# Performance work log

Measured on AMD Instinct MI355X. Metric: run time of the kernel, lower is better.

The kernel has to match this reference:

```python
import jax, jax.numpy as jnp
import numpy as np

B, L, D, H1, OUT, MAX_W = 16, 128, 768, 770, 40, 30


def _span_mask():
    # valid spans: i <= j and width < MAX_W (structured sparsity over the L x L grid)
    ii, jj = np.meshgrid(np.arange(L), np.arange(L), indexing='ij')
    return ((jj >= ii) & (jj - ii < MAX_W)).astype(np.int32)


def setup_inputs():
    key = jax.random.key(0)
    ks = jax.random.split(key, 5)
    hidden_states = jax.random.normal(ks[0], (B, L + 1, D), dtype=jnp.float32)
    rng = np.random.default_rng(0)
    starts = rng.integers(0, L - MAX_W, size=(B,))
    ends = starts + rng.integers(0, MAX_W, size=(B,))
    pred_spans = jnp.asarray(np.stack([starts, ends], axis=1), dtype=jnp.int32)
    span_mask = jnp.asarray(_span_mask())
    W1 = 0.02 * jax.random.normal(ks[1], (2 * D + 1, H1), dtype=jnp.float32)
    b1 = jax.random.normal(ks[2], (H1,), dtype=jnp.float32)
    W2 = 0.02 * jax.random.normal(ks[3], (H1, OUT), dtype=jnp.float32)
    b2 = jax.random.normal(ks[4], (OUT,), dtype=jnp.float32)
    return dict(hidden_states=hidden_states, pred_spans=pred_spans, token_num=L,
                span_available_indication_matrix=span_mask,
                W1=W1, b1=b1, W2=W2, b2=b2)


def reference(hidden_states, pred_spans, token_num, span_available_indication_matrix, W1, b1, W2, b2):
    # span mask is an integer constant -> resolve valid (i, j) pairs on host
    mask = np.asarray(span_available_indication_matrix)
    vi, vj = np.nonzero(mask == 1)            # [n_valid] each
    vi_j = jnp.asarray(vi)
    vj_j = jnp.asarray(vj)
    vecs = hidden_states[:, 1:token_num + 1, :]  # token t -> hidden[:, t+1, :], [B, L, D]
    xi = vecs[:, vi_j, :]                        # [B, n_valid, D] gather of span-start vecs
    xj = vecs[:, vj_j, :]                        # [B, n_valid, D] gather of span-end vecs
    # pred_indications: 2 if span == pred span; 1 if strictly inside it (i<=j); else 0
    s = pred_spans[:, 0:1]
    e = pred_spans[:, 1:2]
    i_ = vi_j[None, :]
    j_ = vj_j[None, :]
    exact = (i_ == s) & (j_ == e)
    inside = (i_ >= s) & (j_ <= e) & (i_ <= j_)
    ind = jnp.where(exact, 2.0, jnp.where(inside, 1.0, 0.0)).astype(hidden_states.dtype)  # [B, n_valid]
    # Linear over concat([xi, xj, ind]) expressed as split matmuls (avoids materializing concat)
    W1i, W1j, w1c = W1[:D], W1[D:2 * D], W1[2 * D]
    h = (jnp.einsum('bnd,dh->bnh', xi, W1i)
         + jnp.einsum('bnd,dh->bnh', xj, W1j)
         + ind[..., None] * w1c + b1)
    h = jax.nn.relu(h)
    logits = jnp.einsum('bnh,ho->bno', h, W2) + b2   # [B, n_valid, OUT]
    return jax.nn.log_softmax(logits, axis=-1)
```

## Files before the change

kernel.cpp:

```cpp
#include <hip/hip_runtime.h>
#include <math.h>

#define B_ 16
#define L_ 128
#define D_ 768
#define H1_ 770
#define OUT_ 40
#define NPAIRS 3405
#define NLOG 1540
#define YSB 1552
#define VOFFB 776
#define KPAD 800
#define W1TROWS 1600
#define NKS 25
#define NTILES 252
#define BSWZ_N (26 * 3 * 512)

#define NB_X 1536
#define NB_W 166
#define NB_T 1200
#define NB_A (NB_X + NB_W + NB_T)
#define NB_B 800
#define NB_C (NTILES * 16)

typedef __attribute__((ext_vector_type(8))) short bf16x8;
typedef __attribute__((ext_vector_type(8))) unsigned short u16x8;
typedef __attribute__((ext_vector_type(4))) float f32x4;
typedef __attribute__((ext_vector_type(4))) unsigned int u32x4;

__device__ inline unsigned short f2bf(float f) {
  unsigned int u = __builtin_bit_cast(unsigned int, f);
  u += 0x7fffu + ((u >> 16) & 1u);
  return (unsigned short)(u >> 16);
}
__device__ inline float bf2f(unsigned short x) {
  return __builtin_bit_cast(float, (unsigned int)x << 16);
}

#if __has_builtin(__builtin_amdgcn_cvt_pk_bf16_f32)
typedef __attribute__((ext_vector_type(2))) __bf16 bf16x2_t;
__device__ inline unsigned int pack_bf16(float lo, float hi) {
  bf16x2_t r = __builtin_amdgcn_cvt_pk_bf16_f32(lo, hi);
  return __builtin_bit_cast(unsigned int, r);
}
#else
__device__ inline unsigned int pack_bf16(float lo, float hi) {
  return (unsigned int)f2bf(lo) | ((unsigned int)f2bf(hi) << 16);
}
#endif

typedef const __attribute__((address_space(1))) void* gas_t;
typedef __attribute__((address_space(3))) void* las_t;
__device__ inline void gl2lds16(const void* g, void* l) {
  __builtin_amdgcn_global_load_lds((gas_t)g, (las_t)l, 16, 0, 0);
}

__device__ inline void tile_decode(int T, int& ti, int& d) {
  if (T < 216) { ti = T / 9; d = T - ti * 9; }
  else {
    int m = T - 216; int r = 24, w = 8;
    while (m >= w) { m -= w; --w; ++r; }
    ti = r; d = m;
  }
}
__device__ inline int pair_rank(int i, int j) {
  return (i < 99) ? i * 30 + (j - i)
                  : NPAIRS - (128 - i) * (129 - i) / 2 + (j - i);
}

__global__ __launch_bounds__(256) void prep_k(
    const float* __restrict__ hidden, const float* __restrict__ W1,
    const float* __restrict__ b1, const float* __restrict__ W2,
    unsigned short* __restrict__ Xb, unsigned short* __restrict__ W1T,
    unsigned short* __restrict__ Bswz, float* __restrict__ Cv)
{
  __shared__ float t[32][33];
  const int u = blockIdx.x;
  const int tid = threadIdx.x;

  if (u < NB_X) {
    int idx = u * 256 + tid;
    int m = idx / 192;
    int c = idx - m * 192;
    float4 f = *(const float4*)(hidden + (size_t)(m + (m >> 7) + 1) * D_ + c * 4);
    ushort4 o;
    o.x = f2bf(f.x); o.y = f2bf(f.y); o.z = f2bf(f.z); o.w = f2bf(f.w);
    *(ushort4*)(Xb + (size_t)m * D_ + c * 4) = o;
  } else if (u < NB_X + NB_W) {
    int idx = (u - NB_X) * 256 + tid;
    if (idx < BSWZ_N) {
      int ks = idx / 1536;
      int rem = idx - ks * 1536;
      int f = rem / 512;
      int l = (rem - f * 512) >> 3;
      int e = rem & 7;
      int n = f * 16 + (l & 15);
      int k = ks * 32 + (l >> 4) * 8 + e;
      float v = (n < OUT_ && k < H1_) ? W2[k * OUT_ + n] : 0.f;
      Bswz[idx] = f2bf(v);
    } else if (idx < BSWZ_N + 3 * KPAD) {
      int c = idx - BSWZ_N;
      int tt = c / KPAD, k = c - tt * KPAD;
      const float* w1c = W1 + 1536 * H1_;
      Cv[c] = (k < H1_) ? (b1[k] + (float)tt * w1c[k]) : 0.f;
    }
  } else {
    int bx = u - NB_X - NB_W;
    const int tx = tid & 31, ty = tid >> 5;
    const int n0 = (bx % 50) * 32, k0 = (bx / 50) * 32;
    #pragma unroll
    for (int r = 0; r < 4; ++r) {
      int k = k0 + ty + r * 8, n = n0 + tx;
      float v = 0.f;
      if (n < H1_)       v = W1[k * H1_ + n];
      else if (n < NLOG) v = W1[(D_ + k) * H1_ + (n - H1_)];
      t[ty + r * 8][tx] = v;
    }
    __syncthreads();
    #pragma unroll
    for (int r = 0; r < 4; ++r) {
      int n = n0 + ty + r * 8, k = k0 + tx;
      W1T[(size_t)n * D_ + k] = f2bf(t[tx][ty + r * 8]);
    }
  }
}

__global__ __launch_bounds__(256) void gemm_k(
    const unsigned short* __restrict__ Xb, const unsigned short* __restrict__ W1T,
    unsigned short* __restrict__ Yb)
{
  __shared__ unsigned short As[64][64];
  __shared__ unsigned short Bs[64][64];
  const int tid = threadIdx.x;
  const int lane = tid & 63, w = tid >> 6;
  const int lm = lane & 15, q = lane >> 4;
  const int xcd = blockIdx.x & 7;
  const int t = blockIdx.x >> 3;
  const int col0 = (t % 25) * 64;
  const int row0 = (xcd * 4 + t / 25) * 64;
  const int m0 = (w >> 1) * 32, n0 = (w & 1) * 32;

  const int srow = w * 16 + (lane >> 3);
  const int schunk = (((lane & 7) ^ ((lane >> 3) & 7))) * 8;
  const unsigned short* ga = Xb  + (size_t)(row0 + srow) * D_ + schunk;
  const unsigned short* gb = W1T + (size_t)(col0 + srow) * D_ + schunk;

  const int xs = lm & 7;

  f32x4 acc[2][2] = {};

  for (int k0 = 0; k0 < D_; k0 += 64) {
    gl2lds16(ga + k0,          &As[w * 16][0]);
    gl2lds16(ga + k0 + 8 * D_, &As[w * 16 + 8][0]);
    gl2lds16(gb + k0,          &Bs[w * 16][0]);
    gl2lds16(gb + k0 + 8 * D_, &Bs[w * 16 + 8][0]);
    __syncthreads();
    #pragma unroll
    for (int ks = 0; ks < 2; ++ks) {
      const int cc = ((ks * 4 + q) ^ xs) * 8;
      bf16x8 a0 = *(const bf16x8*)&As[m0 + lm]     [cc];
      bf16x8 a1 = *(const bf16x8*)&As[m0 + 16 + lm][cc];
      bf16x8 b0 = *(const bf16x8*)&Bs[n0 + lm]     [cc];
      bf16x8 b1 = *(const bf16x8*)&Bs[n0 + 16 + lm][cc];
      acc[0][0] = __builtin_amdgcn_mfma_f32_16x16x32_bf16(a0, b0, acc[0][0], 0, 0, 0);
      acc[0][1] = __builtin_amdgcn_mfma_f32_16x16x32_bf16(a0, b1, acc[0][1], 0, 0, 0);
      acc[1][0] = __builtin_amdgcn_mfma_f32_16x16x32_bf16(a1, b0, acc[1][0], 0, 0, 0);
      acc[1][1] = __builtin_amdgcn_mfma_f32_16x16x32_bf16(a1, b1, acc[1][1], 0, 0, 0);
    }
    __syncthreads();
  }

  #pragma unroll
  for (int ti = 0; ti < 2; ++ti) {
    #pragma unroll
    for (int tj = 0; tj < 2; ++tj) {
      int col = col0 + n0 + tj * 16 + lm;
      if (col >= NLOG) continue;
      int pc = (col < H1_) ? col : col + (VOFFB - H1_);
      #pragma unroll
      for (int r = 0; r < 4; ++r) {
        int row = row0 + m0 + ti * 16 + q * 4 + r;
        Yb[(size_t)row * YSB + pc] = f2bf(acc[ti][tj][r]);
      }
    }
  }
}

__global__ __launch_bounds__(64) void pair_k(
    const unsigned short* __restrict__ Yb, const int* __restrict__ spans,
    const unsigned short* __restrict__ Bswz, const float* __restrict__ Cv,
    const float* __restrict__ b2, float* __restrict__ out)
{
  const int tid = threadIdx.x;
  const int u = blockIdx.x;
  const int bb = u & 15;
  const int T = u >> 4;
  const int lm = tid & 15, q = tid >> 4;

  int ti, d;
  tile_decode(T, ti, d);
  const int i0 = ti * 4, j0 = (ti + d) * 4;

  const int ai = i0 + (lm & 3);
  const int aj = j0 + (lm >> 2);
  const int s = spans[2 * bb], e = spans[2 * bb + 1];
  const int ind = (ai == s && aj == e) ? 2 : ((ai >= s && aj <= e) ? 1 : 0);

  const unsigned short* uptr = Yb + (size_t)(bb * L_ + ai) * YSB + q * 8;
  const unsigned short* vptr = Yb + (size_t)(bb * L_ + aj) * YSB + VOFFB + q * 8;
  const float* cptr = Cv + ind * KPAD + q * 8;
  const unsigned short* bbase = Bswz + tid * 8;

  f32x4 acc0 = {}, acc1 = {}, acc2 = {};

  u16x8 uu0 = *(const u16x8*)(uptr);
  u16x8 vv0 = *(const u16x8*)(vptr);
  u16x8 uu1 = *(const u16x8*)(uptr + 32);
  u16x8 vv1 = *(const u16x8*)(vptr + 32);
  bf16x8 nb0 = *(const bf16x8*)(bbase + 0 * 512);
  bf16x8 nb1 = *(const bf16x8*)(bbase + 1 * 512);
  bf16x8 nb2 = *(const bf16x8*)(bbase + 2 * 512);

  #pragma unroll 5
  for (int ks = 0; ks < NKS; ++ks) {
    const int ko = ks * 32;
    u16x8 cu = uu0, cw = vv0;
    uu0 = uu1; vv0 = vv1;
    uu1 = *(const u16x8*)(uptr + ko + 64);
    vv1 = *(const u16x8*)(vptr + ko + 64);
    bf16x8 b0 = nb0, b1v = nb1, b2f = nb2;
    nb0 = *(const bf16x8*)(bbase + (size_t)(ks * 3 + 3) * 512);
    nb1 = *(const bf16x8*)(bbase + (size_t)(ks * 3 + 4) * 512);
    nb2 = *(const bf16x8*)(bbase + (size_t)(ks * 3 + 5) * 512);
    float4 c0 = *(const float4*)(cptr + ko);
    float4 c1 = *(const float4*)(cptr + ko + 4);
    float h0 = fmaxf(bf2f(cu[0]) + bf2f(cw[0]) + c0.x, 0.f);
    float h1 = fmaxf(bf2f(cu[1]) + bf2f(cw[1]) + c0.y, 0.f);
    float h2 = fmaxf(bf2f(cu[2]) + bf2f(cw[2]) + c0.z, 0.f);
    float h3 = fmaxf(bf2f(cu[3]) + bf2f(cw[3]) + c0.w, 0.f);
    float h4 = fmaxf(bf2f(cu[4]) + bf2f(cw[4]) + c1.x, 0.f);
    float h5 = fmaxf(bf2f(cu[5]) + bf2f(cw[5]) + c1.y, 0.f);
    float h6 = fmaxf(bf2f(cu[6]) + bf2f(cw[6]) + c1.z, 0.f);
    float h7 = fmaxf(bf2f(cu[7]) + bf2f(cw[7]) + c1.w, 0.f);
    u32x4 hp;
    hp[0] = pack_bf16(h0, h1);
    hp[1] = pack_bf16(h2, h3);
    hp[2] = pack_bf16(h4, h5);
    hp[3] = pack_bf16(h6, h7);
    bf16x8 a = __builtin_bit_cast(bf16x8, hp);
    acc0 = __builtin_amdgcn_mfma_f32_16x16x32_bf16(a, b0, acc0, 0, 0, 0);
    acc1 = __builtin_amdgcn_mfma_f32_16x16x32_bf16(a, b1v, acc1, 0, 0, 0);
    acc2 = __builtin_amdgcn_mfma_f32_16x16x32_bf16(a, b2f, acc2, 0, 0, 0);
  }

  const float b2v0 = b2[lm];
  const float b2v1 = b2[16 + lm];
  const float b2v2 = (lm < 8) ? b2[32 + lm] : 0.f;

  #pragma unroll
  for (int r = 0; r < 4; ++r) {
    float l0 = acc0[r] + b2v0;
    float l1 = acc1[r] + b2v1;
    float l2 = (lm < 8) ? (acc2[r] + b2v2) : -INFINITY;
    float mx = fmaxf(fmaxf(l0, l1), l2);
    mx = fmaxf(mx, __shfl_xor(mx, 1));
    mx = fmaxf(mx, __shfl_xor(mx, 2));
    mx = fmaxf(mx, __shfl_xor(mx, 4));
    mx = fmaxf(mx, __shfl_xor(mx, 8));
    float sm = expf(l0 - mx) + expf(l1 - mx) + ((lm < 8) ? expf(l2 - mx) : 0.f);
    sm += __shfl_xor(sm, 1);
    sm += __shfl_xor(sm, 2);
    sm += __shfl_xor(sm, 4);
    sm += __shfl_xor(sm, 8);
    float lsd = mx + logf(sm);

    int pi_ = i0 + r, pj_ = j0 + q;
    if (pj_ >= pi_ && (pj_ - pi_) < 30) {
      float* op = out + ((size_t)bb * NPAIRS + pair_rank(pi_, pj_)) * OUT_;
      op[lm]      = l0 - lsd;
      op[16 + lm] = l1 - lsd;
      if (lm < 8) op[32 + lm] = l2 - lsd;
    }
  }
}

extern "C" void kernel_launch(void* const* d_in, const int* in_sizes, int n_in,
                              void* d_out, int out_size, void* d_ws, size_t ws_size,
                              hipStream_t stream) {
  const float* hidden = (const float*)d_in[0];
  const int*   spans  = (const int*)d_in[1];
  const float* W1 = (const float*)d_in[4];
  const float* b1 = (const float*)d_in[5];
  const float* W2 = (const float*)d_in[6];
  const float* b2 = (const float*)d_in[7];
  float* out = (float*)d_out;

  char* base = (char*)d_ws;
  size_t off = 0;
  auto take = [&](size_t bytes) {
    char* p = base + off;
    off = (off + bytes + 255) & ~(size_t)255;
    return p;
  };
  unsigned short* Yb   = (unsigned short*)take((size_t)2049 * YSB * 2);
  unsigned short* Xb   = (unsigned short*)take((size_t)2048 * D_ * 2);
  unsigned short* W1T  = (unsigned short*)take((size_t)W1TROWS * D_ * 2);
  unsigned short* Bswz = (unsigned short*)take((size_t)BSWZ_N * 2);
  float*          Cv   = (float*)take((size_t)3 * KPAD * 4);

  prep_k<<<dim3(NB_A), 256, 0, stream>>>(hidden, W1, b1, W2, Xb, W1T, Bswz, Cv);
  gemm_k<<<dim3(NB_B), 256, 0, stream>>>(Xb, W1T, Yb);
  pair_k<<<dim3(NB_C), 64, 0, stream>>>(Yb, spans, Bswz, Cv, b2, out);
}
```

Before: 119.6 us.

## Stage W2 fragments in LDS shared by eight-wave pair blocks

Restructures pair_k from 64-thread single-wave blocks into 512-thread blocks of eight waves, covering 2 batches x 4 tiles. Each block copies the swizzled W2 B-fragments (about 76KB) into LDS once with global_load_lds, so the waves read them from shared memory instead of each re-reading them from global/L2. The hidden-activation math is also rewritten with packed 2-wide float ops. The large LDS footprint limits blocks per CU, and the upfront copy plus barrier adds latency before compute starts.

```diff
diff --git a/kernel.cpp b/kernel.cpp
--- a/kernel.cpp
+++ b/kernel.cpp
@@ -21,11 +21,12 @@
 #define NB_T 1200
 #define NB_A (NB_X + NB_W + NB_T)
 #define NB_B 800
-#define NB_C (NTILES * 16)
+#define NB_C (63 * 8)
 
 typedef __attribute__((ext_vector_type(8))) short bf16x8;
 typedef __attribute__((ext_vector_type(8))) unsigned short u16x8;
 typedef __attribute__((ext_vector_type(4))) float f32x4;
+typedef __attribute__((ext_vector_type(2))) float f32x2;
 typedef __attribute__((ext_vector_type(4))) unsigned int u32x4;
 
 __device__ inline unsigned short f2bf(float f) {
@@ -35,6 +36,12 @@
 }
 __device__ inline float bf2f(unsigned short x) {
   return __builtin_bit_cast(float, (unsigned int)x << 16);
+}
+__device__ inline f32x2 unpk_bf(unsigned int d) {
+  f32x2 r;
+  r[0] = __builtin_bit_cast(float, d << 16);
+  r[1] = __builtin_bit_cast(float, d & 0xffff0000u);
+  return r;
 }
 
 #if __has_builtin(__builtin_amdgcn_cvt_pk_bf16_f32)
@@ -186,16 +193,22 @@
   }
 }
 
-__global__ __launch_bounds__(64) void pair_k(
+__global__ __launch_bounds__(512) void pair_k(
     const unsigned short* __restrict__ Yb, const int* __restrict__ spans,
     const unsigned short* __restrict__ Bswz, const float* __restrict__ Cv,
     const float* __restrict__ b2, float* __restrict__ out)
 {
+  __shared__ unsigned short Blds[NKS * 3 * 512];
   const int tid = threadIdx.x;
+  const int w = tid >> 6;
+  const int lane = tid & 63;
   const int u = blockIdx.x;
-  const int bb = u & 15;
-  const int T = u >> 4;
-  const int lm = tid & 15, q = tid >> 4;
+  const int bb = ((u & 7) << 1) | (w >> 2);
+  const int T = (u >> 3) * 4 + (w & 3);
+  const int lm = lane & 15, q = lane >> 4;
+
+  for (int c = w; c < NKS * 3; c += 8)
+    gl2lds16(Bswz + (size_t)c * 512 + lane * 8, &Blds[c * 512]);
 
   int ti, d;
   tile_decode(T, ti, d);
@@ -209,7 +222,9 @@
   const unsigned short* uptr = Yb + (size_t)(bb * L_ + ai) * YSB + q * 8;
   const unsigned short* vptr = Yb + (size_t)(bb * L_ + aj) * YSB + VOFFB + q * 8;
   const float* cptr = Cv + ind * KPAD + q * 8;
-  const unsigned short* bbase = Bswz + tid * 8;
+  const unsigned short* bbase = Blds + lane * 8;
+
+  __syncthreads();
 
   f32x4 acc0 = {}, acc1 = {}, acc2 = {};
 
@@ -217,9 +232,6 @@
   u16x8 vv0 = *(const u16x8*)(vptr);
   u16x8 uu1 = *(const u16x8*)(uptr + 32);
   u16x8 vv1 = *(const u16x8*)(vptr + 32);
-  bf16x8 nb0 = *(const bf16x8*)(bbase + 0 * 512);
-  bf16x8 nb1 = *(const bf16x8*)(bbase + 1 * 512);
-  bf16x8 nb2 = *(const bf16x8*)(bbase + 2 * 512);
 
   #pragma unroll 5
   for (int ks = 0; ks < NKS; ++ks) {
@@ -228,25 +240,27 @@
     uu0 = uu1; vv0 = vv1;
     uu1 = *(const u16x8*)(uptr + ko + 64);
     vv1 = *(const u16x8*)(vptr + ko + 64);
-    bf16x8 b0 = nb0, b1v = nb1, b2f = nb2;
-    nb0 = *(const bf16x8*)(bbase + (size_t)(ks * 3 + 3) * 512);
-    nb1 = *(const bf16x8*)(bbase + (size_t)(ks * 3 + 4) * 512);
-    nb2 = *(const bf16x8*)(bbase + (size_t)(ks * 3 + 5) * 512);
+    bf16x8 b0  = *(const bf16x8*)(bbase + (size_t)(ks * 3 + 0) * 512);
+    bf16x8 b1v = *(const bf16x8*)(bbase + (size_t)(ks * 3 + 1) * 512);
+    bf16x8 b2f = *(const bf16x8*)(bbase + (size_t)(ks * 3 + 2) * 512);
     float4 c0 = *(const float4*)(cptr + ko);
     float4 c1 = *(const float4*)(cptr + ko + 4);
-    float h0 = fmaxf(bf2f(cu[0]) + bf2f(cw[0]) + c0.x, 0.f);
-    float h1 = fmaxf(bf2f(cu[1]) + bf2f(cw[1]) + c0.y, 0.f);
-    float h2 = fmaxf(bf2f(cu[2]) + bf2f(cw[2]) + c0.z, 0.f);
-    float h3 = fmaxf(bf2f(cu[3]) + bf2f(cw[3]) + c0.w, 0.f);
-    float h4 = fmaxf(bf2f(cu[4]) + bf2f(cw[4]) + c1.x, 0.f);
-    float h5 = fmaxf(bf2f(cu[5]) + bf2f(cw[5]) + c1.y, 0.f);
-    float h6 = fmaxf(bf2f(cu[6]) + bf2f(cw[6]) + c1.z, 0.f);
-    float h7 = fmaxf(bf2f(cu[7]) + bf2f(cw[7]) + c1.w, 0.f);
+    u32x4 cud = __builtin_bit_cast(u32x4, cu);
+    u32x4 cwd = __builtin_bit_cast(u32x4, cw);
+    f32x2 cc01; cc01[0] = c0.x; cc01[1] = c0.y;
+    f32x2 cc23; cc23[0] = c0.z; cc23[1] = c0.w;
+    f32x2 cc45; cc45[0] = c1.x; cc45[1] = c1.y;
+    f32x2 cc67; cc67[0] = c1.z; cc67[1] = c1.w;
+    f32x2 zz = {};
+    f32x2 h01 = __builtin_elementwise_max(unpk_bf(cud[0]) + unpk_bf(cwd[0]) + cc01, zz);
+    f32x2 h23 = __builtin_elementwise_max(unpk_bf(cud[1]) + unpk_bf(cwd[1]) + cc23, zz);
+    f32x2 h45 = __builtin_elementwise_max(unpk_bf(cud[2]) + unpk_bf(cwd[2]) + cc45, zz);
+    f32x2 h67 = __builtin_elementwise_max(unpk_bf(cud[3]) + unpk_bf(cwd[3]) + cc67, zz);
     u32x4 hp;
-    hp[0] = pack_bf16(h0, h1);
-    hp[1] = pack_bf16(h2, h3);
-    hp[2] = pack_bf16(h4, h5);
-    hp[3] = pack_bf16(h6, h7);
+    hp[0] = pack_bf16(h01[0], h01[1]);
+    hp[1] = pack_bf16(h23[0], h23[1]);
+    hp[2] = pack_bf16(h45[0], h45[1]);
+    hp[3] = pack_bf16(h67[0], h67[1]);
     bf16x8 a = __builtin_bit_cast(bf16x8, hp);
     acc0 = __builtin_amdgcn_mfma_f32_16x16x32_bf16(a, b0, acc0, 0, 0, 0);
     acc1 = __builtin_amdgcn_mfma_f32_16x16x32_bf16(a, b1v, acc1, 0, 0, 0);
@@ -310,5 +324,5 @@
 
   prep_k<<<dim3(NB_A), 256, 0, stream>>>(hidden, W1, b1, W2, Xb, W1T, Bswz, Cv);
   gemm_k<<<dim3(NB_B), 256, 0, stream>>>(Xb, W1T, Yb);
-  pair_k<<<dim3(NB_C), 64, 0, stream>>>(Yb, spans, Bswz, Cv, b2, out);
-}
+  pair_k<<<dim3(NB_C), 512, 0, stream>>>(Yb, spans, Bswz, Cv, b2, out);
+}
```

Measured after the change: 114.0 us, median of 2. 1.05x faster.
